# Kernel tuning notes

Measured on AMD Instinct MI355X. Metric: run time of the kernel, lower is better.

The kernel has to match this reference:

```python
import jax, jax.numpy as jnp
import numpy as np

FEAT = 320        # in_channel == out_channel, LayerNorm dim
NPTS = 2048       # num_points == Conv1d channels (proj_dim)
TEMP = FEAT ** 0.5
EPS = 1e-5


def setup_inputs() -> dict:
    key = jax.random.key(0)
    ks = jax.random.split(key, 7)
    B = 32
    query = jax.random.normal(ks[0], (B, FEAT, NPTS), dtype=jnp.float32)
    support = jax.random.normal(ks[1], (B, FEAT, NPTS), dtype=jnp.float32)
    # Conv1d(2048, 2048, 1, bias=False) weights, squeezed to [out, in]
    s = 1.0 / np.sqrt(NPTS)
    Wq = jax.random.uniform(ks[2], (NPTS, NPTS), jnp.float32, -s, s)
    Wk = jax.random.uniform(ks[3], (NPTS, NPTS), jnp.float32, -s, s)
    Wv = jax.random.uniform(ks[4], (NPTS, NPTS), jnp.float32, -s, s)
    gamma = jnp.ones((FEAT,), jnp.float32)
    beta = jnp.zeros((FEAT,), jnp.float32)
    return {"query": query, "support": support, "Wq": Wq, "Wk": Wk,
            "Wv": Wv, "gamma": gamma, "beta": beta}


def reference(query, support, Wq, Wk, Wv, gamma, beta):
    # query, support: [B, FEAT=320, NPTS=2048]
    # 1x1 Conv1d on x.transpose(1,2) -> q[b,o,l] = sum_i W[o,i] * x[b,l,i]
    q = jnp.einsum('oi,bfi->bof', Wq, support)   # [B, NPTS, FEAT]
    k = jnp.einsum('oi,bfi->bof', Wk, query)     # [B, NPTS, FEAT]
    v = jnp.einsum('oi,bfi->bof', Wv, query)     # [B, NPTS, FEAT]
    # attn[b,l,m] = sum_o q[b,o,l] * k[b,o,m] / sqrt(FEAT)
    attn = jnp.einsum('bol,bom->blm', q, k) / TEMP   # [B, FEAT, FEAT]
    attn = jax.nn.softmax(attn, axis=-1)
    # query_output[b,l,o] = sum_m attn[b,l,m] * v[b,o,m]
    query_output = jnp.einsum('blm,bom->blo', attn, v)  # [B, FEAT, NPTS]
    # residual + LayerNorm over the FEAT (=320) axis
    up = (query_output + query).transpose(0, 2, 1)      # [B, NPTS, FEAT]
    mu = jnp.mean(up, axis=-1, keepdims=True)
    var = jnp.var(up, axis=-1, keepdims=True)
    normed = (up - mu) * jax.lax.rsqrt(var + EPS) * gamma + beta
    return normed.transpose(0, 2, 1)                    # [B, FEAT, NPTS]
```

## Files before the change

kernel.cpp:

```cpp
#include <hip/hip_runtime.h>

typedef _Float16 f16;
typedef _Float16 f16x4 __attribute__((ext_vector_type(4)));
typedef _Float16 f16x8 __attribute__((ext_vector_type(8)));
typedef float    f32x4 __attribute__((ext_vector_type(4)));

#define NB    32
#define FEAT  320
#define NPTS  2048
#define M1    (NB * FEAT)
#define KDIM  2048

__device__ __forceinline__ void stage16(f16* lds_base, const f16* g) {
    __builtin_amdgcn_global_load_lds(
        (const __attribute__((address_space(1))) void*)g,
        (__attribute__((address_space(3))) void*)lds_base, 16, 0, 0);
}

__global__ void cast_k(const float* __restrict__ src, f16* __restrict__ dst, int n4) {
    int i = blockIdx.x * blockDim.x + threadIdx.x;
    int stride = gridDim.x * blockDim.x;
    for (; i < n4; i += stride) {
        f32x4 v = *(const f32x4*)(src + (size_t)i * 4);
        *(f16x4*)(dst + (size_t)i * 4) = __builtin_convertvector(v, f16x4);
    }
}

__global__ void castT_k(const float* __restrict__ Wq, const float* __restrict__ Wk,
                        f16* __restrict__ WqT, f16* __restrict__ WkT) {
    __shared__ float T[64][65];
    const float* W = blockIdx.z ? Wk : Wq;
    f16* WT        = blockIdx.z ? WkT : WqT;
    const int i0 = blockIdx.x * 64, o0 = blockIdx.y * 64;
    const int tid = threadIdx.x;
#pragma unroll
    for (int j = 0; j < 4; ++j) {
        int e = j * 256 + tid, r = e >> 4, c4 = e & 15;
        f32x4 v = *(const f32x4*)&W[(size_t)(o0 + r) * 2048 + i0 + c4 * 4];
        *(f32x4*)&T[r][c4 * 4] = v;
    }
    __syncthreads();
#pragma unroll
    for (int j = 0; j < 2; ++j) {
        int e = j * 256 + tid, ir = e >> 3, oc8 = e & 7;
        f16x8 val;
#pragma unroll
        for (int k = 0; k < 8; ++k) val[k] = (f16)T[oc8 * 8 + k][ir];
        *(f16x8*)&WT[(size_t)(i0 + ir) * 2048 + o0 + oc8 * 8] = val;
    }
}

__global__ void cast_q_dual(const float* __restrict__ q, f16* __restrict__ qf16,
                            f16* __restrict__ qT16) {
    __shared__ float T[64][65];
    const int b = blockIdx.z;
    const int j0 = blockIdx.x * 64, m0 = blockIdx.y * 64;
    const int tid = threadIdx.x;
#pragma unroll
    for (int j = 0; j < 4; ++j) {
        int e = j * 256 + tid, r = e >> 4, c4 = e & 15;
        size_t src = ((size_t)b * FEAT + m0 + r) * NPTS + j0 + c4 * 4;
        f32x4 v = *(const f32x4*)&q[src];
        *(f32x4*)&T[r][c4 * 4] = v;
        *(f16x4*)&qf16[src] = __builtin_convertvector(v, f16x4);
    }
    __syncthreads();
#pragma unroll
    for (int j = 0; j < 2; ++j) {
        int e = j * 256 + tid, jr = e >> 3, mc8 = e & 7;
        f16x8 val;
#pragma unroll
        for (int k = 0; k < 8; ++k) val[k] = (f16)T[mc8 * 8 + k][jr];
        *(f16x8*)&qT16[((size_t)b * NPTS + j0 + jr) * FEAT + m0 + mc8 * 8] = val;
    }
}

__global__ __launch_bounds__(256, 2) void gemm128_f16(
    const f16* __restrict__ A, const f16* __restrict__ B, f16* __restrict__ C,
    float scale) {
    __shared__ f16 As[2 * 128 * 32];
    __shared__ f16 Bs[2 * 128 * 32];
    const int tid = threadIdx.x, lane = tid & 63, w = tid >> 6;
    const int wm = w >> 1, wn = w & 1, lo = lane & 15, q4 = lane >> 4;
    const long tm = (long)blockIdx.y * 128, tn = (long)blockIdx.x * 128;
    const f16* Abase = A + tm * KDIM;
    const f16* Bbase = B + tn * KDIM;
    f32x4 acc[4][4] = {};
    const int srow = lane >> 2, sch = (lane & 3) * 8;

    for (int k0 = 0; k0 < KDIM; k0 += 64) {
#pragma unroll
        for (int j = 0; j < 4; ++j) {
            const int u = w * 4 + j, h = u & 1, Rb = u >> 1;
            const int base = h * 4096 + Rb * 512;
            const long grow = Rb * 16 + srow;
            const long gk = k0 + h * 32 + sch;
            stage16(&As[base], Abase + grow * KDIM + gk);
            stage16(&Bs[base], Bbase + grow * KDIM + gk);
        }
        __syncthreads();
        f16x8 af[4][2], bf[4][2];
#pragma unroll
        for (int s = 0; s < 2; ++s) {
#pragma unroll
            for (int mi = 0; mi < 4; ++mi)
                af[mi][s] = *(const f16x8*)&As[s * 4096 + (wm * 64 + mi * 16 + lo) * 32 + q4 * 8];
#pragma unroll
            for (int ni = 0; ni < 4; ++ni)
                bf[ni][s] = *(const f16x8*)&Bs[s * 4096 + (wn * 64 + ni * 16 + lo) * 32 + q4 * 8];
        }
#pragma unroll
        for (int s = 0; s < 2; ++s)
#pragma unroll
            for (int mi = 0; mi < 4; ++mi)
#pragma unroll
                for (int ni = 0; ni < 4; ++ni)
                    acc[mi][ni] = __builtin_amdgcn_mfma_f32_16x16x32_f16(af[mi][s], bf[ni][s], acc[mi][ni], 0, 0, 0);
        __syncthreads();
    }
#pragma unroll
    for (int mi = 0; mi < 4; ++mi)
#pragma unroll
        for (int ni = 0; ni < 4; ++ni) {
            long gc = tn + wn * 64 + ni * 16 + lo;
#pragma unroll
            for (int r = 0; r < 4; ++r) {
                long gr = tm + wm * 64 + mi * 16 + q4 * 4 + r;
                C[gr * KDIM + gc] = (f16)(acc[mi][ni][r] * scale);
            }
        }
}

template<int RES>
__global__ __launch_bounds__(512, 2) void gemm_big(
    const f16* __restrict__ A, const f16* __restrict__ B,
    const float* __restrict__ resid, void* __restrict__ outp) {
    __shared__ f16 As[2][320 * 64];
    __shared__ f16 Bs[2][256 * 64];
    const int tid = threadIdx.x, lane = tid & 63, w = tid >> 6;
    const int wm = w >> 2, wn = w & 3, lo = lane & 15, q4 = lane >> 4;
    const int key = lo & 7;
    const long bm0 = (long)blockIdx.y * 320, bn0 = (long)blockIdx.x * 256;
    const int r8 = lane >> 3, sw = (lane & 7) ^ r8;
    const f16* srcA = A + (bm0 + r8) * KDIM + sw * 8;
    const f16* srcB = B + (bn0 + r8) * KDIM + sw * 8;
    const int rA = (wm * 160 + lo) * 64;
    const int rB = (wn * 64 + lo) * 64;
    const int sl0 = (q4 ^ key) * 8;
    const int sl1 = ((q4 | 4) ^ key) * 8;

    f32x4 acc[10][4] = {};

#pragma unroll
    for (int i = 0; i < 5; ++i)
        stage16(&As[0][(w + 8 * i) * 512], srcA + (long)(w + 8 * i) * (8 * KDIM));
#pragma unroll
    for (int i = 0; i < 4; ++i)
        stage16(&Bs[0][(w + 8 * i) * 512], srcB + (long)(w + 8 * i) * (8 * KDIM));
    asm volatile("s_waitcnt vmcnt(0)" ::: "memory");
    __builtin_amdgcn_s_barrier();
    asm volatile("" ::: "memory");

    for (int t = 0; t < KDIM / 64; ++t) {
        const int cur = t & 1, nb = cur ^ 1;
        const long k0n = (long)(t + 1) * 64;
        const bool pf = (t + 1 < KDIM / 64);
        const f16* a = As[cur];
        const f16* b = Bs[cur];
        f16x8 af[5], bf[4];
#pragma unroll
        for (int ni = 0; ni < 4; ++ni) bf[ni] = *(const f16x8*)&b[rB + ni * 1024 + sl0];
#pragma unroll
        for (int i = 0; i < 5; ++i) af[i] = *(const f16x8*)&a[rA + i * 1024 + sl0];
        if (pf) {
#pragma unroll
            for (int i = 0; i < 3; ++i)
                stage16(&As[nb][(w + 8 * i) * 512], srcA + (long)(w + 8 * i) * (8 * KDIM) + k0n);
        }
        __builtin_amdgcn_s_barrier();
        __builtin_amdgcn_s_setprio(1);
#pragma unroll
        for (int i = 0; i < 5; ++i)
#pragma unroll
            for (int ni = 0; ni < 4; ++ni)
                acc[i][ni] = __builtin_amdgcn_mfma_f32_16x16x32_f16(af[i], bf[ni], acc[i][ni], 0, 0, 0);
        __builtin_amdgcn_s_setprio(0);
        __builtin_amdgcn_s_barrier();
#pragma unroll
        for (int i = 0; i < 5; ++i) af[i] = *(const f16x8*)&a[rA + (5 + i) * 1024 + sl0];
        if (pf) {
#pragma unroll
            for (int i = 3; i < 5; ++i)
                stage16(&As[nb][(w + 8 * i) * 512], srcA + (long)(w + 8 * i) * (8 * KDIM) + k0n);
        }
        __builtin_amdgcn_s_barrier();
        __builtin_amdgcn_s_setprio(1);
#pragma unroll
        for (int i = 0; i < 5; ++i)
#pragma unroll
            for (int ni = 0; ni < 4; ++ni)
                acc[5 + i][ni] = __builtin_amdgcn_mfma_f32_16x16x32_f16(af[i], bf[ni], acc[5 + i][ni], 0, 0, 0);
        __builtin_amdgcn_s_setprio(0);
        __builtin_amdgcn_s_barrier();
#pragma unroll
        for (int ni = 0; ni < 4; ++ni) bf[ni] = *(const f16x8*)&b[rB + ni * 1024 + sl1];
#pragma unroll
        for (int i = 0; i < 5; ++i) af[i] = *(const f16x8*)&a[rA + i * 1024 + sl1];
        if (pf) {
#pragma unroll
            for (int i = 0; i < 4; ++i)
                stage16(&Bs[nb][(w + 8 * i) * 512], srcB + (long)(w + 8 * i) * (8 * KDIM) + k0n);
        }
        __builtin_amdgcn_s_barrier();
        __builtin_amdgcn_s_setprio(1);
#pragma unroll
        for (int i = 0; i < 5; ++i)
#pragma unroll
            for (int ni = 0; ni < 4; ++ni)
                acc[i][ni] = __builtin_amdgcn_mfma_f32_16x16x32_f16(af[i], bf[ni], acc[i][ni], 0, 0, 0);
        __builtin_amdgcn_s_setprio(0);
        __builtin_amdgcn_s_barrier();
#pragma unroll
        for (int i = 0; i < 5; ++i) af[i] = *(const f16x8*)&a[rA + (5 + i) * 1024 + sl1];
        __builtin_amdgcn_s_barrier();
        __builtin_amdgcn_s_setprio(1);
#pragma unroll
        for (int i = 0; i < 5; ++i)
#pragma unroll
            for (int ni = 0; ni < 4; ++ni)
                acc[5 + i][ni] = __builtin_amdgcn_mfma_f32_16x16x32_f16(af[i], bf[ni], acc[5 + i][ni], 0, 0, 0);
        __builtin_amdgcn_s_setprio(0);
        asm volatile("s_waitcnt vmcnt(0)" ::: "memory");
        __builtin_amdgcn_s_barrier();
        asm volatile("" ::: "memory");
    }

#pragma unroll
    for (int mi = 0; mi < 10; ++mi)
#pragma unroll
        for (int ni = 0; ni < 4; ++ni) {
            const long gc = bn0 + wn * 64 + ni * 16 + lo;
            const long gr0 = bm0 + wm * 160 + mi * 16 + q4 * 4;
            if (RES) {
                float* out = (float*)outp;
#pragma unroll
                for (int r = 0; r < 4; ++r) {
                    size_t idx = (size_t)(gr0 + r) * KDIM + gc;
                    out[idx] = acc[mi][ni][r] + resid[idx];
                }
            } else {
                f16* out = (f16*)outp;
#pragma unroll
                for (int r = 0; r < 4; ++r)
                    out[(size_t)(gr0 + r) * KDIM + gc] = (f16)acc[mi][ni][r];
            }
        }
}

__global__ __launch_bounds__(256, 2) void attn_gemm(
    const f16* __restrict__ T, const f16* __restrict__ qf16, float* __restrict__ attn) {
    __shared__ f16 As[2 * 64 * 32];
    __shared__ f16 Bs[2 * 64 * 32];
    const int b = blockIdx.z;
    const long tl = (long)blockIdx.y * 64, tmm = (long)blockIdx.x * 64;
    const int tid = threadIdx.x, lane = tid & 63, w = tid >> 6;
    const int wm = w >> 1, wn = w & 1, lo = lane & 15, q4 = lane >> 4;
    const f16* Abase = T + ((long)b * FEAT + tl) * KDIM;
    const f16* Bbase = qf16 + ((long)b * FEAT + tmm) * KDIM;
    const int srow = lane >> 2, sch = (lane & 3) * 8;
    f32x4 acc[2][2] = {};
    for (int k0 = 0; k0 < KDIM; k0 += 64) {
#pragma unroll
        for (int j = 0; j < 2; ++j) {
            const int u = w * 2 + j, h = u & 1, Rb = u >> 1;
            const int base = h * 2048 + Rb * 512;
            const long grow = Rb * 16 + srow;
            const long gk = k0 + h * 32 + sch;
            stage16(&As[base], Abase + grow * KDIM + gk);
            stage16(&Bs[base], Bbase + grow * KDIM + gk);
        }
        __syncthreads();
        f16x8 af[2][2], bf[2][2];
#pragma unroll
        for (int s = 0; s < 2; ++s) {
#pragma unroll
            for (int mi = 0; mi < 2; ++mi)
                af[mi][s] = *(const f16x8*)&As[s * 2048 + (wm * 32 + mi * 16 + lo) * 32 + q4 * 8];
#pragma unroll
            for (int ni = 0; ni < 2; ++ni)
                bf[ni][s] = *(const f16x8*)&Bs[s * 2048 + (wn * 32 + ni * 16 + lo) * 32 + q4 * 8];
        }
#pragma unroll
        for (int s = 0; s < 2; ++s)
#pragma unroll
            for (int mi = 0; mi < 2; ++mi)
#pragma unroll
                for (int ni = 0; ni < 2; ++ni)
                    acc[mi][ni] = __builtin_amdgcn_mfma_f32_16x16x32_f16(af[mi][s], bf[ni][s], acc[mi][ni], 0, 0, 0);
        __syncthreads();
    }
#pragma unroll
    for (int mi = 0; mi < 2; ++mi)
#pragma unroll
        for (int ni = 0; ni < 2; ++ni) {
            long gm = tmm + wn * 32 + ni * 16 + lo;
#pragma unroll
            for (int r = 0; r < 4; ++r) {
                long gl = tl + wm * 32 + mi * 16 + q4 * 4 + r;
                attn[(long)b * (FEAT * FEAT) + gl * FEAT + gm] = acc[mi][ni][r];
            }
        }
}

__global__ __launch_bounds__(256, 2) void u_gemm(
    const f16* __restrict__ P, const f16* __restrict__ qT16, f16* __restrict__ U) {
    __shared__ f16 As[2 * 64 * 32];
    __shared__ f16 Bs[2 * 128 * 32];
    const int b = blockIdx.z;
    const long tl = (long)blockIdx.y * 64, to = (long)blockIdx.x * 128;
    const int tid = threadIdx.x, lane = tid & 63, w = tid >> 6;
    const int wm = w >> 1, wn = w & 1, lo = lane & 15, q4 = lane >> 4;
    const f16* Abase = P + ((long)b * FEAT + tl) * FEAT;
    const f16* Bbase = qT16 + ((long)b * NPTS + to) * FEAT;
    const int srow = lane >> 2, sch = (lane & 3) * 8;
    f32x4 acc[2][4] = {};
    for (int k0 = 0; k0 < FEAT; k0 += 64) {
#pragma unroll
        for (int j = 0; j < 2; ++j) {
            const int u = w * 2 + j, h = u & 1, Rb = u >> 1;
            stage16(&As[h * 2048 + Rb * 512],
                    Abase + (long)(Rb * 16 + srow) * FEAT + k0 + h * 32 + sch);
        }
#pragma unroll
        for (int j = 0; j < 4; ++j) {
            const int u = w * 4 + j, h = u & 1, Rb = u >> 1;
            stage16(&Bs[h * 4096 + Rb * 512],
                    Bbase + (long)(Rb * 16 + srow) * FEAT + k0 + h * 32 + sch);
        }
        __syncthreads();
        f16x8 af[2][2], bf[4][2];
#pragma unroll
        for (int s = 0; s < 2; ++s) {
#pragma unroll
            for (int mi = 0; mi < 2; ++mi)
                af[mi][s] = *(const f16x8*)&As[s * 2048 + (wm * 32 + mi * 16 + lo) * 32 + q4 * 8];
#pragma unroll
            for (int ni = 0; ni < 4; ++ni)
                bf[ni][s] = *(const f16x8*)&Bs[s * 4096 + (wn * 64 + ni * 16 + lo) * 32 + q4 * 8];
        }
#pragma unroll
        for (int s = 0; s < 2; ++s)
#pragma unroll
            for (int mi = 0; mi < 2; ++mi)
#pragma unroll
                for (int ni = 0; ni < 4; ++ni)
                    acc[mi][ni] = __builtin_amdgcn_mfma_f32_16x16x32_f16(af[mi][s], bf[ni][s], acc[mi][ni], 0, 0, 0);
        __syncthreads();
    }
#pragma unroll
    for (int mi = 0; mi < 2; ++mi)
#pragma unroll
        for (int ni = 0; ni < 4; ++ni) {
            long go = to + wn * 64 + ni * 16 + lo;
#pragma unroll
            for (int r = 0; r < 4; ++r) {
                long gl = tl + wm * 32 + mi * 16 + q4 * 4 + r;
                U[((long)b * FEAT + gl) * NPTS + go] = (f16)acc[mi][ni][r];
            }
        }
}

__global__ void softmax_k(const float* __restrict__ attn, f16* __restrict__ probs) {
    const int r = blockIdx.x * 4 + (threadIdx.x >> 6);
    const int lane = threadIdx.x & 63;
    const float* row = attn + (size_t)r * FEAT;
    float v[5];
    float mx = -1e30f;
#pragma unroll
    for (int j = 0; j < 5; ++j) { v[j] = row[lane + j * 64]; mx = fmaxf(mx, v[j]); }
#pragma unroll
    for (int off = 32; off; off >>= 1) mx = fmaxf(mx, __shfl_xor(mx, off, 64));
    float s = 0.f;
#pragma unroll
    for (int j = 0; j < 5; ++j) { v[j] = __expf(v[j] - mx); s += v[j]; }
#pragma unroll
    for (int off = 32; off; off >>= 1) s += __shfl_xor(s, off, 64);
    const float inv = 1.f / s;
    f16* prow = probs + (size_t)r * FEAT;
#pragma unroll
    for (int j = 0; j < 5; ++j) prow[lane + j * 64] = (f16)(v[j] * inv);
}

__global__ void ln_k(float* __restrict__ out, const float* __restrict__ gamma,
                     const float* __restrict__ beta) {
    __shared__ float g[FEAT], bt[FEAT];
    const int tid = threadIdx.x;
    for (int i = tid; i < FEAT; i += 256) { g[i] = gamma[i]; bt[i] = beta[i]; }
    __syncthreads();
    const int col = blockIdx.x * 256 + tid;
    const int b = col >> 11, o = col & 2047;
    float* base = out + (size_t)b * (FEAT * NPTS) + o;
    float s = 0.f, ss = 0.f;
    for (int l = 0; l < FEAT; ++l) {
        float x = base[(size_t)l * NPTS];
        s += x; ss += x * x;
    }
    const float mu = s * (1.f / FEAT);
    const float var = ss * (1.f / FEAT) - mu * mu;
    const float rstd = rsqrtf(var + 1e-5f);
    for (int l = 0; l < FEAT; ++l) {
        float x = base[(size_t)l * NPTS];
        base[(size_t)l * NPTS] = (x - mu) * rstd * g[l] + bt[l];
    }
}

extern "C" void kernel_launch(void* const* d_in, const int* in_sizes, int n_in,
                              void* d_out, int out_size, void* d_ws, size_t ws_size,
                              hipStream_t stream) {
    const float* query   = (const float*)d_in[0];
    const float* support = (const float*)d_in[1];
    const float* Wq      = (const float*)d_in[2];
    const float* Wk      = (const float*)d_in[3];
    const float* Wv      = (const float*)d_in[4];
    const float* gamma   = (const float*)d_in[5];
    const float* beta    = (const float*)d_in[6];
    float* out = (float*)d_out;

    char* ws = (char*)d_ws;
    const size_t SZ_W = (size_t)KDIM * KDIM * sizeof(f16);
    const size_t SZ_X = (size_t)M1 * KDIM * sizeof(f16);
    f16* wqT  = (f16*)(ws);
    f16* wkT  = (f16*)(ws + SZ_W);
    f16* wv16 = (f16*)(ws + 2 * SZ_W);
    f16* gt   = (f16*)(ws + 3 * SZ_W);
    f16* sf16 = (f16*)(ws + 4 * SZ_W);
    f16* qf16 = (f16*)(ws + 4 * SZ_W + SZ_X);
    f16* qT16 = (f16*)(ws + 4 * SZ_W + 2 * SZ_X);
    f16* T    = (f16*)(ws + 4 * SZ_W + 3 * SZ_X);
    float* attn = (float*)(ws);
    f16*   P    = qf16;
    f16*   U    = sf16;

    const float inv_temp = 0.05590169943749474f;

    castT_k<<<dim3(32, 32, 2), 256, 0, stream>>>(Wq, Wk, wqT, wkT);
    cast_k<<<1024, 256, 0, stream>>>(Wv, wv16, (KDIM * KDIM) / 4);
    cast_k<<<2048, 256, 0, stream>>>(support, sf16, (M1 * KDIM) / 4);
    cast_q_dual<<<dim3(32, 5, 32), 256, 0, stream>>>(query, qf16, qT16);

    gemm128_f16<<<dim3(16, 16), 256, 0, stream>>>(wkT, wqT, gt, inv_temp);
    gemm_big<0><<<dim3(8, 32), 512, 0, stream>>>(sf16, gt, nullptr, T);
    attn_gemm<<<dim3(5, 5, 32), 256, 0, stream>>>(T, qf16, attn);
    softmax_k<<<2560, 256, 0, stream>>>(attn, P);
    u_gemm<<<dim3(16, 5, 32), 256, 0, stream>>>(P, qT16, U);
    gemm_big<1><<<dim3(8, 32), 512, 0, stream>>>(U, wv16, query, out);
    ln_k<<<256, 256, 0, stream>>>(out, gamma, beta);
}
```

Baseline: 681.5 us.

## Reorder A/B prefetch staging by consumption order with partial vmcnt waits

Reassigns which A-tile row strips each wave stages so that strips needed first, the upper half with sl0 and sl1 k-chunks, arrive early. B is now prefetched first. Full vmcnt(0) drains are replaced with partial waits at two points in the iteration, so some loads stay in flight across the tile boundary instead of stalling at the end of every k-step. The risk is subtle ordering bugs. The per-wave strip mapping must correctly cover all 40 strips, and the vmcnt counts must match the number of outstanding loads.

```diff
diff --git a/kernel.cpp b/kernel.cpp
--- a/kernel.cpp
+++ b/kernel.cpp
@@ -140,6 +140,7 @@
     const int tid = threadIdx.x, lane = tid & 63, w = tid >> 6;
     const int wm = w >> 2, wn = w & 3, lo = lane & 15, q4 = lane >> 4;
     const int key = lo & 7;
+    const int wu = __builtin_amdgcn_readfirstlane(w);
     const long bm0 = (long)blockIdx.y * 320, bn0 = (long)blockIdx.x * 256;
     const int r8 = lane >> 3, sw = (lane & 7) ^ r8;
     const f16* srcA = A + (bm0 + r8) * KDIM + sw * 8;
@@ -149,15 +150,37 @@
     const int sl0 = (q4 ^ key) * 8;
     const int sl1 = ((q4 | 4) ^ key) * 8;
 
+    int a_str[5], nA0;
+    if (wu < 4) {
+        nA0 = 3;
+        const int b0 = 3 * wu;
+        a_str[0] = (b0     < 10) ? b0     : b0 + 10;
+        a_str[1] = (b0 + 1 < 10) ? b0 + 1 : b0 + 11;
+        a_str[2] = (b0 + 2 < 10) ? b0 + 2 : b0 + 12;
+        const int c0 = 2 * wu;
+        a_str[3] = c0 + 10;
+        a_str[4] = c0 + 11;
+    } else {
+        nA0 = 2;
+        const int b0 = 12 + 2 * (wu - 4);
+        a_str[0] = b0 + 10;
+        a_str[1] = b0 + 11;
+        const int c0 = 8 + 3 * (wu - 4);
+        a_str[2] = (c0     < 10) ? c0 + 10 : c0 + 20;
+        a_str[3] = (c0 + 1 < 10) ? c0 + 11 : c0 + 21;
+        a_str[4] = (c0 + 2 < 10) ? c0 + 12 : c0 + 22;
+    }
+
     f32x4 acc[10][4] = {};
 
-#pragma unroll
-    for (int i = 0; i < 5; ++i)
-        stage16(&As[0][(w + 8 * i) * 512], srcA + (long)(w + 8 * i) * (8 * KDIM));
 #pragma unroll
     for (int i = 0; i < 4; ++i)
         stage16(&Bs[0][(w + 8 * i) * 512], srcB + (long)(w + 8 * i) * (8 * KDIM));
-    asm volatile("s_waitcnt vmcnt(0)" ::: "memory");
+#pragma unroll
+    for (int i = 0; i < 5; ++i)
+        stage16(&As[0][a_str[i] * 512], srcA + (long)a_str[i] * (8 * KDIM));
+    if (wu < 4) asm volatile("s_waitcnt vmcnt(2)" ::: "memory");
+    else        asm volatile("s_waitcnt vmcnt(3)" ::: "memory");
     __builtin_amdgcn_s_barrier();
     asm volatile("" ::: "memory");
 
@@ -174,8 +197,8 @@
         for (int i = 0; i < 5; ++i) af[i] = *(const f16x8*)&a[rA + i * 1024 + sl0];
         if (pf) {
 #pragma unroll
-            for (int i = 0; i < 3; ++i)
-                stage16(&As[nb][(w + 8 * i) * 512], srcA + (long)(w + 8 * i) * (8 * KDIM) + k0n);
+            for (int i = 0; i < 4; ++i)
+                stage16(&Bs[nb][(w + 8 * i) * 512], srcB + (long)(w + 8 * i) * (8 * KDIM) + k0n);
         }
         __builtin_amdgcn_s_barrier();
         __builtin_amdgcn_s_setprio(1);
@@ -185,13 +208,17 @@
             for (int ni = 0; ni < 4; ++ni)
                 acc[i][ni] = __builtin_amdgcn_mfma_f32_16x16x32_f16(af[i], bf[ni], acc[i][ni], 0, 0, 0);
         __builtin_amdgcn_s_setprio(0);
-        __builtin_amdgcn_s_barrier();
+        if (pf) asm volatile("s_waitcnt vmcnt(4)" ::: "memory");
+        else    asm volatile("s_waitcnt vmcnt(0)" ::: "memory");
+        __builtin_amdgcn_s_barrier();
+        asm volatile("" ::: "memory");
 #pragma unroll
         for (int i = 0; i < 5; ++i) af[i] = *(const f16x8*)&a[rA + (5 + i) * 1024 + sl0];
         if (pf) {
 #pragma unroll
-            for (int i = 3; i < 5; ++i)
-                stage16(&As[nb][(w + 8 * i) * 512], srcA + (long)(w + 8 * i) * (8 * KDIM) + k0n);
+            for (int i = 0; i < 5; ++i)
+                if (i < nA0)
+                    stage16(&As[nb][a_str[i] * 512], srcA + (long)a_str[i] * (8 * KDIM) + k0n);
         }
         __builtin_amdgcn_s_barrier();
         __builtin_amdgcn_s_setprio(1);
@@ -208,8 +235,9 @@
         for (int i = 0; i < 5; ++i) af[i] = *(const f16x8*)&a[rA + i * 1024 + sl1];
         if (pf) {
 #pragma unroll
-            for (int i = 0; i < 4; ++i)
-                stage16(&Bs[nb][(w + 8 * i) * 512], srcB + (long)(w + 8 * i) * (8 * KDIM) + k0n);
+            for (int i = 0; i < 5; ++i)
+                if (i >= nA0)
+                    stage16(&As[nb][a_str[i] * 512], srcA + (long)a_str[i] * (8 * KDIM) + k0n);
         }
         __builtin_amdgcn_s_barrier();
         __builtin_amdgcn_s_setprio(1);
@@ -230,9 +258,12 @@
             for (int ni = 0; ni < 4; ++ni)
                 acc[5 + i][ni] = __builtin_amdgcn_mfma_f32_16x16x32_f16(af[i], bf[ni], acc[5 + i][ni], 0, 0, 0);
         __builtin_amdgcn_s_setprio(0);
-        asm volatile("s_waitcnt vmcnt(0)" ::: "memory");
-        __builtin_amdgcn_s_barrier();
-        asm volatile("" ::: "memory");
+        if (pf) {
+            if (wu < 4) asm volatile("s_waitcnt vmcnt(2)" ::: "memory");
+            else        asm volatile("s_waitcnt vmcnt(3)" ::: "memory");
+            __builtin_amdgcn_s_barrier();
+            asm volatile("" ::: "memory");
+        }
     }
 
 #pragma unroll
```

Result: faster. 661.8 us (-2.9%).

## Fuse LayerNorm into final GEMM epilogue, shrink GEMM tile, merge cast kernels

Applied to the files above, without the earlier changes.

The big GEMM tile changes from 320x256 to 320x128, doubling the grid to 512 blocks. Its inner loop is simplified to one barrier per k-step, with the whole next tile prefetched up front and both k-halves loaded before the MFMAs. The residual-GEMM epilogue now computes LayerNorm statistics over the 320-row block with cross-wave LDS reduction and writes normalized output, which removes the separate ln_k pass that re-read and re-wrote the full fp32 output. The two fp32-to-f16 cast launches are merged into one. The smaller tile reuses data less per block and the single-barrier schedule may overlap less, but the change cuts memory traffic and launches.

```diff
diff --git a/kernel.cpp b/kernel.cpp
--- a/kernel.cpp
+++ b/kernel.cpp
@@ -17,12 +17,19 @@
         (__attribute__((address_space(3))) void*)lds_base, 16, 0, 0);
 }
 
-__global__ void cast_k(const float* __restrict__ src, f16* __restrict__ dst, int n4) {
+__global__ void cast2_k(const float* __restrict__ a, f16* __restrict__ da, int n4a,
+                        const float* __restrict__ b, f16* __restrict__ db, int n4b) {
     int i = blockIdx.x * blockDim.x + threadIdx.x;
     int stride = gridDim.x * blockDim.x;
-    for (; i < n4; i += stride) {
-        f32x4 v = *(const f32x4*)(src + (size_t)i * 4);
-        *(f16x4*)(dst + (size_t)i * 4) = __builtin_convertvector(v, f16x4);
+    for (; i < n4a + n4b; i += stride) {
+        if (i < n4a) {
+            f32x4 v = *(const f32x4*)(a + (size_t)i * 4);
+            *(f16x4*)(da + (size_t)i * 4) = __builtin_convertvector(v, f16x4);
+        } else {
+            size_t j = (size_t)(i - n4a);
+            f32x4 v = *(const f32x4*)(b + j * 4);
+            *(f16x4*)(db + j * 4) = __builtin_convertvector(v, f16x4);
+        }
     }
 }
 
@@ -134,29 +141,36 @@
 template<int RES>
 __global__ __launch_bounds__(512, 2) void gemm_big(
     const f16* __restrict__ A, const f16* __restrict__ B,
-    const float* __restrict__ resid, void* __restrict__ outp) {
+    const float* __restrict__ resid, void* __restrict__ outp,
+    const float* __restrict__ gamma, const float* __restrict__ beta) {
     __shared__ f16 As[2][320 * 64];
-    __shared__ f16 Bs[2][256 * 64];
+    __shared__ f16 Bs[2][128 * 64];
+    __shared__ float lnbuf[4][128][2];
+    __shared__ float gb[2][FEAT];
     const int tid = threadIdx.x, lane = tid & 63, w = tid >> 6;
-    const int wm = w >> 2, wn = w & 3, lo = lane & 15, q4 = lane >> 4;
+    const int wm = w >> 1, wn = w & 1, lo = lane & 15, q4 = lane >> 4;
     const int key = lo & 7;
-    const long bm0 = (long)blockIdx.y * 320, bn0 = (long)blockIdx.x * 256;
+    const long bm0 = (long)blockIdx.y * 320, bn0 = (long)blockIdx.x * 128;
     const int r8 = lane >> 3, sw = (lane & 7) ^ r8;
     const f16* srcA = A + (bm0 + r8) * KDIM + sw * 8;
     const f16* srcB = B + (bn0 + r8) * KDIM + sw * 8;
-    const int rA = (wm * 160 + lo) * 64;
+    const int rA = (wm * 80 + lo) * 64;
     const int rB = (wn * 64 + lo) * 64;
     const int sl0 = (q4 ^ key) * 8;
     const int sl1 = ((q4 | 4) ^ key) * 8;
 
-    f32x4 acc[10][4] = {};
-
+    f32x4 acc[5][4] = {};
+
+    if (RES) {
+        for (int i = tid; i < FEAT; i += 512) { gb[0][i] = gamma[i]; gb[1][i] = beta[i]; }
+    }
+
+#pragma unroll
+    for (int i = 0; i < 2; ++i)
+        stage16(&Bs[0][(w + 8 * i) * 512], srcB + (long)(w + 8 * i) * (8 * KDIM));
 #pragma unroll
     for (int i = 0; i < 5; ++i)
         stage16(&As[0][(w + 8 * i) * 512], srcA + (long)(w + 8 * i) * (8 * KDIM));
-#pragma unroll
-    for (int i = 0; i < 4; ++i)
-        stage16(&Bs[0][(w + 8 * i) * 512], srcB + (long)(w + 8 * i) * (8 * KDIM));
     asm volatile("s_waitcnt vmcnt(0)" ::: "memory");
     __builtin_amdgcn_s_barrier();
     asm volatile("" ::: "memory");
@@ -165,96 +179,118 @@
         const int cur = t & 1, nb = cur ^ 1;
         const long k0n = (long)(t + 1) * 64;
         const bool pf = (t + 1 < KDIM / 64);
+        if (pf) {
+#pragma unroll
+            for (int i = 0; i < 2; ++i)
+                stage16(&Bs[nb][(w + 8 * i) * 512], srcB + (long)(w + 8 * i) * (8 * KDIM) + k0n);
+#pragma unroll
+            for (int i = 0; i < 5; ++i)
+                stage16(&As[nb][(w + 8 * i) * 512], srcA + (long)(w + 8 * i) * (8 * KDIM) + k0n);
+        }
         const f16* a = As[cur];
         const f16* b = Bs[cur];
-        f16x8 af[5], bf[4];
-#pragma unroll
-        for (int ni = 0; ni < 4; ++ni) bf[ni] = *(const f16x8*)&b[rB + ni * 1024 + sl0];
-#pragma unroll
-        for (int i = 0; i < 5; ++i) af[i] = *(const f16x8*)&a[rA + i * 1024 + sl0];
+        f16x8 af0[5], af1[5], bf0[4], bf1[4];
+#pragma unroll
+        for (int ni = 0; ni < 4; ++ni) bf0[ni] = *(const f16x8*)&b[rB + ni * 1024 + sl0];
+#pragma unroll
+        for (int i = 0; i < 5; ++i)    af0[i] = *(const f16x8*)&a[rA + i * 1024 + sl0];
+#pragma unroll
+        for (int ni = 0; ni < 4; ++ni) bf1[ni] = *(const f16x8*)&b[rB + ni * 1024 + sl1];
+#pragma unroll
+        for (int i = 0; i < 5; ++i)    af1[i] = *(const f16x8*)&a[rA + i * 1024 + sl1];
+        __builtin_amdgcn_s_setprio(1);
+#pragma unroll
+        for (int i = 0; i < 5; ++i)
+#pragma unroll
+            for (int ni = 0; ni < 4; ++ni)
+                acc[i][ni] = __builtin_amdgcn_mfma_f32_16x16x32_f16(af0[i], bf0[ni], acc[i][ni], 0, 0, 0);
+        __builtin_amdgcn_s_setprio(0);
+        __builtin_amdgcn_s_setprio(1);
+#pragma unroll
+        for (int i = 0; i < 5; ++i)
+#pragma unroll
+            for (int ni = 0; ni < 4; ++ni)
+                acc[i][ni] = __builtin_amdgcn_mfma_f32_16x16x32_f16(af1[i], bf1[ni], acc[i][ni], 0, 0, 0);
+        __builtin_amdgcn_s_setprio(0);
         if (pf) {
-#pragma unroll
-            for (int i = 0; i < 3; ++i)
-                stage16(&As[nb][(w + 8 * i) * 512], srcA + (long)(w + 8 * i) * (8 * KDIM) + k0n);
-        }
-        __builtin_amdgcn_s_barrier();
-        __builtin_amdgcn_s_setprio(1);
-#pragma unroll
-        for (int i = 0; i < 5; ++i)
+            asm volatile("s_waitcnt vmcnt(0)" ::: "memory");
+            __builtin_amdgcn_s_barrier();
+            asm volatile("" ::: "memory");
+        }
+    }
+
+    if (RES) {
+        float* out = (float*)outp;
+#pragma unroll
+        for (int mi = 0; mi < 5; ++mi)
+#pragma unroll
+            for (int ni = 0; ni < 4; ++ni) {
+                const long gc = bn0 + wn * 64 + ni * 16 + lo;
+                const long gr0 = bm0 + wm * 80 + mi * 16 + q4 * 4;
+#pragma unroll
+                for (int r = 0; r < 4; ++r)
+                    acc[mi][ni][r] += resid[(size_t)(gr0 + r) * KDIM + gc];
+            }
+        float s[4] = {}, ss[4] = {};
+#pragma unroll
+        for (int mi = 0; mi < 5; ++mi)
 #pragma unroll
             for (int ni = 0; ni < 4; ++ni)
-                acc[i][ni] = __builtin_amdgcn_mfma_f32_16x16x32_f16(af[i], bf[ni], acc[i][ni], 0, 0, 0);
-        __builtin_amdgcn_s_setprio(0);
-        __builtin_amdgcn_s_barrier();
-#pragma unroll
-        for (int i = 0; i < 5; ++i) af[i] = *(const f16x8*)&a[rA + (5 + i) * 1024 + sl0];
-        if (pf) {
-#pragma unroll
-            for (int i = 3; i < 5; ++i)
-                stage16(&As[nb][(w + 8 * i) * 512], srcA + (long)(w + 8 * i) * (8 * KDIM) + k0n);
-        }
-        __builtin_amdgcn_s_barrier();
-        __builtin_amdgcn_s_setprio(1);
-#pragma unroll
-        for (int i = 0; i < 5; ++i)
-#pragma unroll
-            for (int ni = 0; ni < 4; ++ni)
-                acc[5 + i][ni] = __builtin_amdgcn_mfma_f32_16x16x32_f16(af[i], bf[ni], acc[5 + i][ni], 0, 0, 0);
-        __builtin_amdgcn_s_setprio(0);
-        __builtin_amdgcn_s_barrier();
-#pragma unroll
-        for (int ni = 0; ni < 4; ++ni) bf[ni] = *(const f16x8*)&b[rB + ni * 1024 + sl1];
-#pragma unroll
-        for (int i = 0; i < 5; ++i) af[i] = *(const f16x8*)&a[rA + i * 1024 + sl1];
-        if (pf) {
-#pragma unroll
-            for (int i = 0; i < 4; ++i)
-                stage16(&Bs[nb][(w + 8 * i) * 512], srcB + (long)(w + 8 * i) * (8 * KDIM) + k0n);
-        }
-        __builtin_amdgcn_s_barrier();
-        __builtin_amdgcn_s_setprio(1);
-#pragma unroll
-        for (int i = 0; i < 5; ++i)
-#pragma unroll
-            for (int ni = 0; ni < 4; ++ni)
-                acc[i][ni] = __builtin_amdgcn_mfma_f32_16x16x32_f16(af[i], bf[ni], acc[i][ni], 0, 0, 0);
-        __builtin_amdgcn_s_setprio(0);
-        __builtin_amdgcn_s_barrier();
-#pragma unroll
-        for (int i = 0; i < 5; ++i) af[i] = *(const f16x8*)&a[rA + (5 + i) * 1024 + sl1];
-        __builtin_amdgcn_s_barrier();
-        __builtin_amdgcn_s_setprio(1);
-#pragma unroll
-        for (int i = 0; i < 5; ++i)
-#pragma unroll
-            for (int ni = 0; ni < 4; ++ni)
-                acc[5 + i][ni] = __builtin_amdgcn_mfma_f32_16x16x32_f16(af[i], bf[ni], acc[5 + i][ni], 0, 0, 0);
-        __builtin_amdgcn_s_setprio(0);
-        asm volatile("s_waitcnt vmcnt(0)" ::: "memory");
-        __builtin_amdgcn_s_barrier();
-        asm volatile("" ::: "memory");
-    }
-
-#pragma unroll
-    for (int mi = 0; mi < 10; ++mi)
+#pragma unroll
+                for (int r = 0; r < 4; ++r) {
+                    float v = acc[mi][ni][r];
+                    s[ni] += v; ss[ni] += v * v;
+                }
 #pragma unroll
         for (int ni = 0; ni < 4; ++ni) {
-            const long gc = bn0 + wn * 64 + ni * 16 + lo;
-            const long gr0 = bm0 + wm * 160 + mi * 16 + q4 * 4;
-            if (RES) {
-                float* out = (float*)outp;
+            s[ni]  += __shfl_xor(s[ni], 16, 64);  s[ni]  += __shfl_xor(s[ni], 32, 64);
+            ss[ni] += __shfl_xor(ss[ni], 16, 64); ss[ni] += __shfl_xor(ss[ni], 32, 64);
+        }
+        if (q4 == 0) {
+#pragma unroll
+            for (int ni = 0; ni < 4; ++ni) {
+                int c = wn * 64 + ni * 16 + lo;
+                lnbuf[wm][c][0] = s[ni];
+                lnbuf[wm][c][1] = ss[ni];
+            }
+        }
+        __syncthreads();
+        float mu[4], rstd[4];
+#pragma unroll
+        for (int ni = 0; ni < 4; ++ni) {
+            int c = wn * 64 + ni * 16 + lo;
+            float S = lnbuf[0][c][0] + lnbuf[1][c][0] + lnbuf[2][c][0] + lnbuf[3][c][0];
+            float SS = lnbuf[0][c][1] + lnbuf[1][c][1] + lnbuf[2][c][1] + lnbuf[3][c][1];
+            mu[ni] = S * (1.0f / FEAT);
+            float var = SS * (1.0f / FEAT) - mu[ni] * mu[ni];
+            rstd[ni] = rsqrtf(var + 1e-5f);
+        }
+#pragma unroll
+        for (int mi = 0; mi < 5; ++mi)
+#pragma unroll
+            for (int ni = 0; ni < 4; ++ni) {
+                const long gc = bn0 + wn * 64 + ni * 16 + lo;
+                const long gr0 = bm0 + wm * 80 + mi * 16 + q4 * 4;
 #pragma unroll
                 for (int r = 0; r < 4; ++r) {
-                    size_t idx = (size_t)(gr0 + r) * KDIM + gc;
-                    out[idx] = acc[mi][ni][r] + resid[idx];
+                    int l = wm * 80 + mi * 16 + q4 * 4 + r;
+                    out[(size_t)(gr0 + r) * KDIM + gc] =
+                        (acc[mi][ni][r] - mu[ni]) * rstd[ni] * gb[0][l] + gb[1][l];
                 }
-            } else {
-                f16* out = (f16*)outp;
+            }
+    } else {
+        f16* out = (f16*)outp;
+#pragma unroll
+        for (int mi = 0; mi < 5; ++mi)
+#pragma unroll
+            for (int ni = 0; ni < 4; ++ni) {
+                const long gc = bn0 + wn * 64 + ni * 16 + lo;
+                const long gr0 = bm0 + wm * 80 + mi * 16 + q4 * 4;
 #pragma unroll
                 for (int r = 0; r < 4; ++r)
                     out[(size_t)(gr0 + r) * KDIM + gc] = (f16)acc[mi][ni][r];
             }
-        }
+    }
 }
 
 __global__ __launch_bounds__(256, 2) void attn_gemm(
@@ -389,29 +425,6 @@
     f16* prow = probs + (size_t)r * FEAT;
 #pragma unroll
     for (int j = 0; j < 5; ++j) prow[lane + j * 64] = (f16)(v[j] * inv);
-}
-
-__global__ void ln_k(float* __restrict__ out, const float* __restrict__ gamma,
-                     const float* __restrict__ beta) {
-    __shared__ float g[FEAT], bt[FEAT];
-    const int tid = threadIdx.x;
-    for (int i = tid; i < FEAT; i += 256) { g[i] = gamma[i]; bt[i] = beta[i]; }
-    __syncthreads();
-    const int col = blockIdx.x * 256 + tid;
-    const int b = col >> 11, o = col & 2047;
-    float* base = out + (size_t)b * (FEAT * NPTS) + o;
-    float s = 0.f, ss = 0.f;
-    for (int l = 0; l < FEAT; ++l) {
-        float x = base[(size_t)l * NPTS];
-        s += x; ss += x * x;
-    }
-    const float mu = s * (1.f / FEAT);
-    const float var = ss * (1.f / FEAT) - mu * mu;
-    const float rstd = rsqrtf(var + 1e-5f);
-    for (int l = 0; l < FEAT; ++l) {
-        float x = base[(size_t)l * NPTS];
-        base[(size_t)l * NPTS] = (x - mu) * rstd * g[l] + bt[l];
-    }
 }
 
 extern "C" void kernel_launch(void* const* d_in, const int* in_sizes, int n_in,
@@ -444,15 +457,14 @@
     const float inv_temp = 0.05590169943749474f;
 
     castT_k<<<dim3(32, 32, 2), 256, 0, stream>>>(Wq, Wk, wqT, wkT);
-    cast_k<<<1024, 256, 0, stream>>>(Wv, wv16, (KDIM * KDIM) / 4);
-    cast_k<<<2048, 256, 0, stream>>>(support, sf16, (M1 * KDIM) / 4);
+    cast2_k<<<2048, 256, 0, stream>>>(Wv, wv16, (KDIM * KDIM) / 4,
+                                      support, sf16, (M1 * KDIM) / 4);
     cast_q_dual<<<dim3(32, 5, 32), 256, 0, stream>>>(query, qf16, qT16);
 
     gemm128_f16<<<dim3(16, 16), 256, 0, stream>>>(wkT, wqT, gt, inv_temp);
-    gemm_big<0><<<dim3(8, 32), 512, 0, stream>>>(sf16, gt, nullptr, T);
+    gemm_big<0><<<dim3(16, 32), 512, 0, stream>>>(sf16, gt, nullptr, T, nullptr, nullptr);
     attn_gemm<<<dim3(5, 5, 32), 256, 0, stream>>>(T, qf16, attn);
     softmax_k<<<2560, 256, 0, stream>>>(attn, P);
     u_gemm<<<dim3(16, 5, 32), 256, 0, stream>>>(P, qT16, U);
-    gemm_big<1><<<dim3(8, 32), 512, 0, stream>>>(U, wv16, query, out);
-    ln_k<<<256, 256, 0, stream>>>(out, gamma, beta);
-}
+    gemm_big<1><<<dim3(16, 32), 512, 0, stream>>>(U, wv16, query, out, gamma, beta);
+}
```

Result: faster. 637.6 us (-6.4%).
